# Kernel optimization log

Hardware: AMD Instinct MI355X
Metric: run time of the kernel (lower is better)

Reference implementation:

```python
import jax, jax.numpy as jnp
import numpy as np

CLASS_NUM = 80
REG_MAX = 16
INPUT_W, INPUT_H = 640, 640
BS, MAXB, TOPK = 16, 20, 10
ALPHA, BETA = 0.5, 6.0
EPS = 1e-9
BOX_W, CLS_W, DFL_W = 7.5, 0.5, 1.5


def _make_anchors(strides=(8, 16, 32), offset=0.5):
    pts, svec = [], []
    for s in strides:
        h, w = INPUT_H // s, INPUT_W // s
        sx = np.arange(w, dtype=np.float32) + offset
        sy = np.arange(h, dtype=np.float32) + offset
        gy, gx = np.meshgrid(sy, sx, indexing="ij")
        pts.append(np.stack([gx, gy], -1).reshape(-1, 2))
        svec.append(np.full((h * w, 1), s, dtype=np.float32))
    return jnp.asarray(np.concatenate(pts)), jnp.asarray(np.concatenate(svec))


def _xywh2xyxy(x):
    xy, wh = x[..., :2], x[..., 2:4]
    return jnp.concatenate([xy - wh / 2, xy + wh / 2], -1)


def _ciou(b1, b2, eps=1e-7):
    # b1, b2: (..., 4) in xyxy; standard ultralytics CIoU (h gets +eps -> safe for zero boxes)
    b1x1, b1y1, b1x2, b1y2 = (b1[..., i] for i in range(4))
    b2x1, b2y1, b2x2, b2y2 = (b2[..., i] for i in range(4))
    w1, h1 = b1x2 - b1x1, b1y2 - b1y1 + eps
    w2, h2 = b2x2 - b2x1, b2y2 - b2y1 + eps
    inter = (jnp.minimum(b1x2, b2x2) - jnp.maximum(b1x1, b2x1)).clip(0) * \
            (jnp.minimum(b1y2, b2y2) - jnp.maximum(b1y1, b2y1)).clip(0)
    union = w1 * h1 + w2 * h2 - inter + eps
    iou = inter / union
    cw = jnp.maximum(b1x2, b2x2) - jnp.minimum(b1x1, b2x1)
    ch = jnp.maximum(b1y2, b2y2) - jnp.minimum(b1y1, b2y1)
    c2 = cw * cw + ch * ch + eps
    rho2 = ((b2x1 + b2x2 - b1x1 - b1x2) ** 2 + (b2y1 + b2y2 - b1y1 - b1y2) ** 2) / 4.0
    v = (4.0 / np.pi ** 2) * (jnp.arctan(w2 / h2) - jnp.arctan(w1 / h1)) ** 2
    alpha = jax.lax.stop_gradient(v / (v - iou + (1.0 + eps)))
    return iou - (rho2 / c2 + v * alpha)


def _assigner(pd_scores, pd_bboxes, anc_points, gt_labels, gt_bboxes, mask_gt):
    # Task-aligned assignment. pd_scores (b,na,nc) sigmoided, pd_bboxes (b,na,4), mask_gt (b,M,1).
    b, na, nc = pd_scores.shape
    M = gt_bboxes.shape[1]
    f32 = pd_scores.dtype
    # anchors whose center lies inside each gt box -> (b,M,na)
    lt = anc_points[None, None] - gt_bboxes[:, :, None, :2]
    rb = gt_bboxes[:, :, None, 2:] - anc_points[None, None]
    mask_in_gts = (jnp.concatenate([lt, rb], -1).min(-1) > EPS).astype(f32)
    mask = mask_in_gts * mask_gt  # (b,M,na)
    labels = gt_labels[..., 0].astype(jnp.int32)  # (b,M)
    idx = jnp.broadcast_to(labels[:, :, None], (b, M, na))
    bbox_scores = jnp.take_along_axis(pd_scores.transpose(0, 2, 1), idx, axis=1) * mask  # (b,M,na)
    overlaps = jnp.clip(_ciou(gt_bboxes[:, :, None, :], pd_bboxes[:, None, :, :]), 0) * mask
    align = bbox_scores ** ALPHA * overlaps ** BETA  # (b,M,na)
    # topk candidates per gt along anchors
    _, topk_idxs = jax.lax.top_k(align, TOPK)  # (b,M,TOPK)
    valid = jnp.broadcast_to(mask_gt > 0, (b, M, TOPK))
    idxs = jnp.where(valid, topk_idxs, 0).reshape(b * M, TOPK)
    cnt = jnp.zeros((b * M, na), f32).at[jnp.arange(b * M)[:, None], idxs].add(
        valid.reshape(b * M, TOPK).astype(f32)).reshape(b, M, na)
    mask_topk = jnp.where(cnt > 1, 0.0, cnt)
    mask_pos = mask_topk * mask  # (b,M,na)
    # anchors claimed by multiple gts keep only the highest-overlap gt
    fg = mask_pos.sum(-2)  # (b,na)
    is_max = jax.nn.one_hot(overlaps.argmax(1), M, dtype=f32).transpose(0, 2, 1)  # (b,M,na)
    mask_pos = jnp.where(fg[:, None, :] > 1, is_max, mask_pos)
    fg_mask = mask_pos.sum(-2)  # (b,na)
    target_gt_idx = mask_pos.argmax(-2)  # (b,na)
    flat_idx = target_gt_idx + jnp.arange(b)[:, None] * M
    t_labels = labels.reshape(-1)[flat_idx]  # (b,na)
    t_bboxes = gt_bboxes.reshape(-1, 4)[flat_idx]  # (b,na,4)
    t_scores = jax.nn.one_hot(t_labels, nc, dtype=f32) * (fg_mask[..., None] > 0).astype(f32)
    # normalize by task-aligned metric
    align = align * mask_pos
    pos_align = align.max(axis=-1, keepdims=True)  # (b,M,1)
    pos_overlaps = (overlaps * mask_pos).max(axis=-1, keepdims=True)
    norm = (align * pos_overlaps / (pos_align + EPS)).max(axis=-2)[..., None]  # (b,na,1)
    return t_bboxes, t_scores * norm, fg_mask


def yolo_loss(feat0, feat1, feat2, annotations):
    rm = REG_MAX
    preds = []
    for f in (feat0, feat1, feat2):
        b, c, h, w = f.shape
        preds.append(f.reshape(b, c, h * w).transpose(0, 2, 1))
    preds = jnp.concatenate(preds, 1)  # (b, 8400, 4*rm+nc)
    pred_regs = preds[..., :4 * rm]
    pred_scores = preds[..., 4 * rm:]
    anc_points, stride_scales = _make_anchors()  # (8400,2), (8400,1)
    b, a, _ = pred_regs.shape
    # DFL decode: softmax over 16 bins, expectation with proj = arange(16)
    dist = jax.nn.softmax(pred_regs.reshape(b, a, 4, rm), -1) @ jnp.arange(rm, dtype=preds.dtype)
    pred_bboxes = jnp.concatenate([anc_points - dist[..., :2], anc_points + dist[..., 2:]], -1)
    # gt processing: fixed MAXB boxes per image, zero padded (ann_process equivalent)
    res = annotations.reshape(b, MAXB, 6)[..., 1:]
    scales = jnp.array([INPUT_W, INPUT_H, INPUT_W, INPUT_H], dtype=res.dtype)
    gt_bboxes = _xywh2xyxy(res[..., :4]) * scales
    gt_labels = res[..., 4:]
    gt_mask = (gt_bboxes.sum(2, keepdims=True) > 0).astype(res.dtype)
    t_bboxes, t_scores, fg_mask = _assigner(
        jax.lax.stop_gradient(jax.nn.sigmoid(pred_scores)),
        jax.lax.stop_gradient(pred_bboxes * stride_scales),
        anc_points * stride_scales, gt_labels, gt_bboxes, gt_mask)
    tss = jnp.maximum(t_scores.sum(), 1.0)
    # cls: BCE-with-logits, sum / target_scores_sum
    x, t = pred_scores, t_scores
    bce = jnp.maximum(x, 0) - x * t + jnp.log1p(jnp.exp(-jnp.abs(x)))
    loss_cls = bce.sum() / tss
    # box (CIoU) + DFL, weighted by per-anchor score sum on fg anchors
    t_bboxes = t_bboxes / stride_scales
    weight = t_scores.sum(-1) * fg_mask  # (b,na); zero off fg
    iou = _ciou(pred_bboxes, t_bboxes)
    loss_box = jnp.sum((1.0 - iou) * weight) / tss
    target_ltrb = jnp.clip(
        jnp.concatenate([anc_points - t_bboxes[..., :2], t_bboxes[..., 2:] - anc_points], -1),
        0.0, (rm - 1) - 0.01)  # (b,na,4)
    logp = jax.nn.log_softmax(pred_regs.reshape(b, a, 4, rm), -1)
    tl = target_ltrb.astype(jnp.int32)
    wl = (tl + 1).astype(logp.dtype) - target_ltrb
    ce_tl = -jnp.take_along_axis(logp, tl[..., None], -1)[..., 0]
    ce_tr = -jnp.take_along_axis(logp, tl[..., None] + 1, -1)[..., 0]
    dfl = (ce_tl * wl + ce_tr * (1.0 - wl)).mean(-1)  # (b,na)
    loss_dfl = jnp.sum(dfl * weight) / tss
    loss = jnp.stack([loss_box * BOX_W, loss_cls * CLS_W, loss_dfl * DFL_W])
    return loss.sum(), jax.lax.stop_gradient(loss)


def setup_inputs() -> dict:
    key = jax.random.key(0)
    k1, k2, k3, k4, k5, k6 = jax.random.split(key, 6)
    C = 4 * REG_MAX + CLASS_NUM  # 144
    feat0 = jax.random.normal(k1, (BS, C, 80, 80), jnp.float32)
    feat1 = jax.random.normal(k2, (BS, C, 40, 40), jnp.float32)
    feat2 = jax.random.normal(k3, (BS, C, 20, 20), jnp.float32)
    # annotations rows: [batch_idx, x, y, w, h (normalized), cls]; zero-padded to MAXB per image
    cx = jax.random.uniform(k4, (BS, MAXB), minval=0.15, maxval=0.85)
    cy = jax.random.uniform(jax.random.fold_in(k4, 1), (BS, MAXB), minval=0.15, maxval=0.85)
    w = jax.random.uniform(k5, (BS, MAXB), minval=0.05, maxval=0.3)
    h = jax.random.uniform(jax.random.fold_in(k5, 1), (BS, MAXB), minval=0.05, maxval=0.3)
    cls = jax.random.randint(k6, (BS, MAXB), 0, CLASS_NUM).astype(jnp.float32)
    counts = jax.random.randint(jax.random.fold_in(k6, 1), (BS,), 5, MAXB + 1)
    valid = (jnp.arange(MAXB)[None, :] < counts[:, None]).astype(jnp.float32)
    bidx = jnp.broadcast_to(jnp.arange(BS, dtype=jnp.float32)[:, None], (BS, MAXB))
    ann = jnp.stack([bidx, cx * valid, cy * valid, w * valid, h * valid, cls * valid], -1)
    return {"feat0": feat0, "feat1": feat1, "feat2": feat2,
            "annotations": ann.reshape(BS * MAXB, 6)}


def reference(feat0, feat1, feat2, annotations):
    return yolo_loss(feat0, feat1, feat2, annotations)
```

## Files before the change

kernel.cpp:

```cpp
#include <hip/hip_runtime.h>

#define NA_TOT 8400
#define A0 6400
#define A1 8000
#define NC_TOT 144
#define BSZ 16
#define MB 20
#define TOPKN 10
#define NCLS 80


__device__ __forceinline__ const float* feat_sel(const float* f0, const float* f1,
                                                 const float* f2, int a, int& hw, int& pos) {
  if (a < A0) { hw = 6400; pos = a;      return f0; }
  if (a < A1) { hw = 1600; pos = a - A0; return f1; }
  hw = 400; pos = a - A1; return f2;
}

__device__ __forceinline__ void anchor_geom(int a, float& stride, float& ax, float& ay) {
  int pos, w;
  if (a < A0)      { pos = a;      w = 80; stride = 8.f;  }
  else if (a < A1) { pos = a - A0; w = 40; stride = 16.f; }
  else             { pos = a - A1; w = 20; stride = 32.f; }
  int y = pos / w, x = pos - y * w;
  ax = (float)x + 0.5f; ay = (float)y + 0.5f;
}

__device__ __forceinline__ float ciou_f(float b1x1, float b1y1, float b1x2, float b1y2,
                                        float b2x1, float b2y1, float b2x2, float b2y2) {
  const float eps = 1e-7f;
  float w1 = b1x2 - b1x1, h1 = b1y2 - b1y1 + eps;
  float w2 = b2x2 - b2x1, h2 = b2y2 - b2y1 + eps;
  float iw = fminf(b1x2, b2x2) - fmaxf(b1x1, b2x1);
  float ih = fminf(b1y2, b2y2) - fmaxf(b1y1, b2y1);
  float inter = fmaxf(iw, 0.f) * fmaxf(ih, 0.f);
  float uni = w1 * h1 + w2 * h2 - inter + eps;
  float iou = inter / uni;
  float cw = fmaxf(b1x2, b2x2) - fminf(b1x1, b2x1);
  float ch = fmaxf(b1y2, b2y2) - fminf(b1y1, b2y1);
  float c2 = cw * cw + ch * ch + eps;
  float dx = b2x1 + b2x2 - b1x1 - b1x2;
  float dy = b2y1 + b2y2 - b1y1 - b1y2;
  float rho2 = (dx * dx + dy * dy) * 0.25f;
  float dat = atanf(w2 / h2) - atanf(w1 / h1);
  float v = 0.4052847345693511f * dat * dat;
  float alpha = v / (v - iou + (1.f + eps));
  return iou - (rho2 / c2 + v * alpha);
}

__device__ __forceinline__ bool better(float v1, int i1, float v2, int i2) {
  return (v1 > v2) || (v1 == v2 && i1 < i2);
}


#define PREP_TILES 132

__global__ __launch_bounds__(256) void k_prep(const float* __restrict__ f0,
                                              const float* __restrict__ f1,
                                              const float* __restrict__ f2,
                                              float4* __restrict__ pbox,
                                              float4* __restrict__ lse4,
                                              double* __restrict__ acc) {
  __shared__ float s_d[64][5];
  __shared__ float s_ls[64][5];
  __shared__ float s_red[4];
  int tile = blockIdx.x % PREP_TILES;
  int b    = blockIdx.x / PREP_TILES;
  int w = threadIdx.x >> 6, l = threadIdx.x & 63;
  int a = tile * 64 + l;
  float bce = 0.f;
  if (a < NA_TOT) {
    int hw, pos; const float* f = feat_sel(f0, f1, f2, a, hw, pos);
    const float* base = f + (size_t)b * NC_TOT * hw + pos;
    float v[16]; float m = -1e30f;
#pragma unroll
    for (int i = 0; i < 16; i++) { v[i] = base[(size_t)(w * 16 + i) * hw]; m = fmaxf(m, v[i]); }
    float s = 0.f, ws = 0.f;
#pragma unroll
    for (int i = 0; i < 16; i++) { float e = expf(v[i] - m); s += e; ws += e * (float)i; }
    s_d[l][w]  = ws / s;
    s_ls[l][w] = m + logf(s);
#pragma unroll
    for (int j = 0; j < 20; j++) {
      float x = base[(size_t)(64 + w * 20 + j) * hw];
      bce += fmaxf(x, 0.f) + log1pf(expf(-fabsf(x)));
    }
  }
  for (int o = 32; o > 0; o >>= 1) bce += __shfl_down(bce, o, 64);
  if (l == 0) s_red[w] = bce;
  __syncthreads();
  if (threadIdx.x == 0)
    atomicAdd(&acc[0], (double)(s_red[0] + s_red[1] + s_red[2] + s_red[3]));
  if (threadIdx.x < 64 && a < NA_TOT) {
    float stride, ax, ay; anchor_geom(a, stride, ax, ay);
    int idx = b * NA_TOT + a;
    pbox[idx] = make_float4(ax - s_d[l][0], ay - s_d[l][1], ax + s_d[l][2], ay + s_d[l][3]);
    lse4[idx] = make_float4(s_ls[l][0], s_ls[l][1], s_ls[l][2], s_ls[l][3]);
  }
}


__global__ __launch_bounds__(256) void k_align(const float* __restrict__ f0,
                                               const float* __restrict__ f1,
                                               const float* __restrict__ f2,
                                               const float* __restrict__ ann,
                                               const float4* __restrict__ pbox,
                                               float* __restrict__ alg,
                                               float* __restrict__ ovl,
                                               unsigned char* __restrict__ sel) {
  int idx = blockIdx.x * 256 + threadIdx.x;
  int bm = idx / NA_TOT, a = idx - bm * NA_TOT;
  int b = bm / MB;
  const float* g = ann + (size_t)bm * 6;
  float cx = g[1], cy = g[2], w_ = g[3], h_ = g[4];
  float gx1 = (cx - w_ * 0.5f) * 640.f, gy1 = (cy - h_ * 0.5f) * 640.f;
  float gx2 = (cx + w_ * 0.5f) * 640.f, gy2 = (cy + h_ * 0.5f) * 640.f;
  int label = (int)g[5];
  bool valid = (gx1 + gy1 + gx2 + gy2) > 0.f;

  float stride, ax, ay; anchor_geom(a, stride, ax, ay);
  float axp = ax * stride, ayp = ay * stride;
  float mn = fminf(fminf(axp - gx1, ayp - gy1), fminf(gx2 - axp, gy2 - ayp));
  float al = 0.f, ov = 0.f;
  if (valid && mn > 1e-9f) {
    float4 pb = pbox[b * NA_TOT + a];
    float px1 = pb.x * stride, py1 = pb.y * stride;
    float px2 = pb.z * stride, py2 = pb.w * stride;
    ov = fmaxf(ciou_f(gx1, gy1, gx2, gy2, px1, py1, px2, py2), 0.f);
    int hw, pos; const float* f = feat_sel(f0, f1, f2, a, hw, pos);
    float xs = f[((size_t)b * NC_TOT + 64 + label) * hw + pos];
    float sg = 1.f / (1.f + expf(-xs));
    float o2 = ov * ov;
    al = sqrtf(sg) * (o2 * o2 * o2);
  }
  alg[idx] = al;
  ovl[idx] = ov;
  sel[idx] = 0;
}


__global__ __launch_bounds__(256) void k_topk(const float* __restrict__ alg,
                                              const float* __restrict__ ann,
                                              unsigned char* __restrict__ sel) {
  __shared__ float s_v[4];
  __shared__ int   s_i[4];
  __shared__ float s_bv;
  __shared__ int   s_bi;
  __shared__ int   s_top[TOPKN];

  int bm = blockIdx.x;
  const float* row = alg + (size_t)bm * NA_TOT;
  const float* g = ann + (size_t)bm * 6;
  float cx = g[1], cy = g[2], w_ = g[3], h_ = g[4];
  float gx1 = (cx - w_ * 0.5f) * 640.f, gy1 = (cy - h_ * 0.5f) * 640.f;
  float gx2 = (cx + w_ * 0.5f) * 640.f, gy2 = (cy + h_ * 0.5f) * 640.f;
  bool valid = (gx1 + gy1 + gx2 + gy2) > 0.f;

  float lv[TOPKN]; int li[TOPKN];
#pragma unroll
  for (int k = 0; k < TOPKN; k++) { lv[k] = -1.f; li[k] = 0x7fffffff; }
  for (int a = threadIdx.x; a < NA_TOT; a += 256) {
    float v = row[a];
    if (better(v, a, lv[TOPKN - 1], li[TOPKN - 1])) {
      float cv = v; int ci = a;
#pragma unroll
      for (int k = 0; k < TOPKN; k++) {
        bool bb = better(cv, ci, lv[k], li[k]);
        float tv = bb ? cv : lv[k]; int ti = bb ? ci : li[k];
        cv = bb ? lv[k] : cv;       ci = bb ? li[k] : ci;
        lv[k] = tv; li[k] = ti;
      }
    }
  }

  int wv = threadIdx.x >> 6;
  for (int k = 0; k < TOPKN; k++) {
    float bv = lv[0]; int bi = li[0];
    for (int o = 32; o > 0; o >>= 1) {
      float xv = __shfl_down(bv, o, 64);
      int   xi = __shfl_down(bi, o, 64);
      if (better(xv, xi, bv, bi)) { bv = xv; bi = xi; }
    }
    if ((threadIdx.x & 63) == 0) { s_v[wv] = bv; s_i[wv] = bi; }
    __syncthreads();
    if (threadIdx.x == 0) {
      float fv = s_v[0]; int fi = s_i[0];
      for (int q = 1; q < 4; q++)
        if (better(s_v[q], s_i[q], fv, fi)) { fv = s_v[q]; fi = s_i[q]; }
      s_top[k] = fi; s_bv = fv; s_bi = fi;
    }
    __syncthreads();
    if (lv[0] == s_bv && li[0] == s_bi) {
#pragma unroll
      for (int q = 0; q < TOPKN - 1; q++) { lv[q] = lv[q + 1]; li[q] = li[q + 1]; }
      lv[TOPKN - 1] = -1.f; li[TOPKN - 1] = 0x7fffffff;
    }
    __syncthreads();
  }

  if (threadIdx.x < TOPKN && valid) {
    int a = s_top[threadIdx.x];
    float stride, ax, ay; anchor_geom(a, stride, ax, ay);
    float axp = ax * stride, ayp = ay * stride;
    float mn = fminf(fminf(axp - gx1, ayp - gy1), fminf(gx2 - axp, gy2 - ayp));
    if (mn > 1e-9f) sel[(size_t)bm * NA_TOT + a] = 1;
  }
}


__global__ __launch_bounds__(256) void k_resolve(const float* __restrict__ alg,
                                                 const float* __restrict__ ovl,
                                                 const unsigned char* __restrict__ sel,
                                                 unsigned char* __restrict__ tgt,
                                                 unsigned char* __restrict__ fgm,
                                                 unsigned int* __restrict__ pos_a,
                                                 unsigned int* __restrict__ pos_o) {
  int idx = blockIdx.x * 256 + threadIdx.x;
  int b = idx / NA_TOT, a = idx - b * NA_TOT;
  size_t col = (size_t)b * MB * NA_TOT + a;
  int fg = 0, first = -1;
#pragma unroll
  for (int m = 0; m < MB; m++) {
    int v = sel[col + (size_t)m * NA_TOT];
    fg += v;
    if (v && first < 0) first = m;
  }
  int t, f;
  if (fg > 1) {
    float bv = ovl[col]; int bm_ = 0;
#pragma unroll
    for (int m = 1; m < MB; m++) {
      float v = ovl[col + (size_t)m * NA_TOT];
      if (v > bv) { bv = v; bm_ = m; }
    }
    t = bm_; f = 1;
  } else {
    t = (first >= 0) ? first : 0;
    f = fg;
  }
  tgt[idx] = (unsigned char)t;
  fgm[idx] = (unsigned char)f;
  if (f) {
    int bm = b * MB + t;
    float al = alg[(size_t)bm * NA_TOT + a];
    float ov = ovl[(size_t)bm * NA_TOT + a];
    atomicMax(&pos_a[bm], __float_as_uint(al));
    atomicMax(&pos_o[bm], __float_as_uint(ov));
  }
}


__global__ __launch_bounds__(256) void k_loss(const float* __restrict__ f0,
                                              const float* __restrict__ f1,
                                              const float* __restrict__ f2,
                                              const float* __restrict__ ann,
                                              const float4* __restrict__ pbox,
                                              const float4* __restrict__ lse4,
                                              const float* __restrict__ alg,
                                              const unsigned char* __restrict__ tgt,
                                              const unsigned char* __restrict__ fgm,
                                              const unsigned int* __restrict__ pos_a,
                                              const unsigned int* __restrict__ pos_o,
                                              double* __restrict__ acc) {
  int idx = blockIdx.x * 256 + threadIdx.x;
  int b = idx / NA_TOT, a = idx - b * NA_TOT;
  float c_cls = 0.f, c_box = 0.f, c_dfl = 0.f, c_tss = 0.f;

  if (fgm[idx]) {
    int t = tgt[idx];
    int bm = b * MB + t;
    float al = alg[(size_t)bm * NA_TOT + a];
    float norm = al * __uint_as_float(pos_o[bm]) / (__uint_as_float(pos_a[bm]) + 1e-9f);

    const float* g = ann + (size_t)bm * 6;
    float stride, ax, ay; anchor_geom(a, stride, ax, ay);
    int hw, pos; const float* f = feat_sel(f0, f1, f2, a, hw, pos);
    const float* base = f + (size_t)b * NC_TOT * hw + pos;

    int label = (int)g[5];
    float xs = base[(size_t)(64 + label) * hw];
    c_cls = xs * norm;
    c_tss = norm;

    float cx = g[1], cy = g[2], w_ = g[3], h_ = g[4];
    float inv = 1.f / stride;
    float tx1 = (cx - w_ * 0.5f) * 640.f * inv, ty1 = (cy - h_ * 0.5f) * 640.f * inv;
    float tx2 = (cx + w_ * 0.5f) * 640.f * inv, ty2 = (cy + h_ * 0.5f) * 640.f * inv;

    float4 pb = pbox[idx];
    float iou = ciou_f(pb.x, pb.y, pb.z, pb.w, tx1, ty1, tx2, ty2);
    c_box = (1.f - iou) * norm;

    float4 ls = lse4[idx];
    float ltv[4] = { ax - tx1, ay - ty1, tx2 - ax, ty2 - ay };
    float lsa[4] = { ls.x, ls.y, ls.z, ls.w };
    float dfl = 0.f;
#pragma unroll
    for (int g4 = 0; g4 < 4; g4++) {
      float tv = fminf(fmaxf(ltv[g4], 0.f), 14.99f);
      int   tl = (int)tv;
      float wl = (float)(tl + 1) - tv;
      float xl = base[(size_t)(g4 * 16 + tl) * hw];
      float xr = base[(size_t)(g4 * 16 + tl + 1) * hw];
      dfl += (lsa[g4] - xl) * wl + (lsa[g4] - xr) * (1.f - wl);
    }
    c_dfl = dfl * 0.25f * norm;
  }

  for (int o = 32; o > 0; o >>= 1) {
    c_cls += __shfl_down(c_cls, o, 64);
    c_box += __shfl_down(c_box, o, 64);
    c_dfl += __shfl_down(c_dfl, o, 64);
    c_tss += __shfl_down(c_tss, o, 64);
  }
  __shared__ float sh[4][4];
  int wv = threadIdx.x >> 6;
  if ((threadIdx.x & 63) == 0) { sh[wv][0] = c_cls; sh[wv][1] = c_box; sh[wv][2] = c_dfl; sh[wv][3] = c_tss; }
  __syncthreads();
  if (threadIdx.x == 0) {
    float t0 = sh[0][0] + sh[1][0] + sh[2][0] + sh[3][0];
    float t1 = sh[0][1] + sh[1][1] + sh[2][1] + sh[3][1];
    float t2 = sh[0][2] + sh[1][2] + sh[2][2] + sh[3][2];
    float t3 = sh[0][3] + sh[1][3] + sh[2][3] + sh[3][3];
    atomicAdd(&acc[0], -(double)t0);
    atomicAdd(&acc[1],  (double)t1);
    atomicAdd(&acc[2],  (double)t2);
    atomicAdd(&acc[3],  (double)t3);
  }
}


__global__ void k_finish(const double* __restrict__ acc, float* __restrict__ out) {
  double tss = acc[3]; if (tss < 1.0) tss = 1.0;
  float lb = (float)(acc[1] / tss) * 7.5f;
  float lc = (float)(acc[0] / tss) * 0.5f;
  float ld = (float)(acc[2] / tss) * 1.5f;
  out[0] = lb + lc + ld;
  out[1] = lb;
  out[2] = lc;
  out[3] = ld;
}


extern "C" void kernel_launch(void* const* d_in, const int* in_sizes, int n_in,
                              void* d_out, int out_size, void* d_ws, size_t ws_size,
                              hipStream_t stream) {
  const float* f0  = (const float*)d_in[0];
  const float* f1  = (const float*)d_in[1];
  const float* f2  = (const float*)d_in[2];
  const float* ann = (const float*)d_in[3];

  char* p = (char*)d_ws;
  size_t off = 0;
  double* acc = (double*)(p + off);               off += 64;
  unsigned int* pos_a = (unsigned int*)(p + off); off += (size_t)BSZ * MB * 4;
  unsigned int* pos_o = (unsigned int*)(p + off); off += (size_t)BSZ * MB * 4;
  size_t zero_bytes = off;
  float4* pbox = (float4*)(p + off);              off += (size_t)BSZ * NA_TOT * 16;
  float4* lse4 = (float4*)(p + off);              off += (size_t)BSZ * NA_TOT * 16;
  float* alg = (float*)(p + off);                 off += (size_t)BSZ * MB * NA_TOT * 4;
  float* ovl = (float*)(p + off);                 off += (size_t)BSZ * MB * NA_TOT * 4;
  unsigned char* sel = (unsigned char*)(p + off); off += (size_t)BSZ * MB * NA_TOT;
  unsigned char* tgt = (unsigned char*)(p + off); off += (size_t)BSZ * NA_TOT;
  unsigned char* fgm = (unsigned char*)(p + off); off += (size_t)BSZ * NA_TOT;

  hipMemsetAsync(acc, 0, zero_bytes, stream);

  const int NBLK = (BSZ * NA_TOT) / 256;
  k_prep<<<BSZ * PREP_TILES, 256, 0, stream>>>(f0, f1, f2, pbox, lse4, acc);
  k_align<<<(BSZ * MB * NA_TOT) / 256, 256, 0, stream>>>(f0, f1, f2, ann, pbox, alg, ovl, sel);
  k_topk<<<BSZ * MB, 256, 0, stream>>>(alg, ann, sel);
  k_resolve<<<NBLK, 256, 0, stream>>>(alg, ovl, sel, tgt, fgm, pos_a, pos_o);
  k_loss<<<NBLK, 256, 0, stream>>>(f0, f1, f2, ann, pbox, lse4, alg, tgt, fgm, pos_a, pos_o, acc);
  k_finish<<<1, 1, 0, stream>>>(acc, (float*)d_out);
}
```

Baseline: 203.1 us.

## Use per-anchor bitmask for top-k selection and precompute GT box terms

Replaces the per-(gt,anchor) byte selection array with a per-anchor 32-bit mask set by atomicOr in top-k, so resolve reads one word and uses popcount/ffs instead of scanning 20 rows. A new tiny kernel precomputes GT box corners, area, atan of aspect, label and validity, which align and top-k then load as two float4s. The BCE sum is rewritten to multiply (1+exp(-|x|)) terms and take one log, using fast __expf. This cuts memory traffic and transcendental work, at the cost of an extra launch, atomics, and a possible overflow or precision change in the product-of-terms BCE.

After: 191.7 us. -5.6%, faster.

```diff
diff --git a/kernel.cpp b/kernel.cpp
--- a/kernel.cpp
+++ b/kernel.cpp
@@ -53,6 +53,22 @@
 }
 
 
+__global__ void k_gtt(const float* __restrict__ ann, float* __restrict__ gtt) {
+  int bm = threadIdx.x;
+  const float* g = ann + bm * 6;
+  float cx = g[1], cy = g[2], w_ = g[3], h_ = g[4];
+  float gx1 = (cx - w_ * 0.5f) * 640.f, gy1 = (cy - h_ * 0.5f) * 640.f;
+  float gx2 = (cx + w_ * 0.5f) * 640.f, gy2 = (cy + h_ * 0.5f) * 640.f;
+  float w1 = gx2 - gx1, h1 = gy2 - gy1 + 1e-7f;
+  float* o = gtt + bm * 8;
+  o[0] = gx1; o[1] = gy1; o[2] = gx2; o[3] = gy2;
+  o[4] = w1 * h1;
+  o[5] = atanf(w1 / h1);
+  o[6] = g[5];
+  o[7] = ((gx1 + gy1 + gx2 + gy2) > 0.f) ? 1.f : 0.f;
+}
+
+
 #define PREP_TILES 132
 
 __global__ __launch_bounds__(256) void k_prep(const float* __restrict__ f0,
@@ -60,10 +76,12 @@
                                               const float* __restrict__ f2,
                                               float4* __restrict__ pbox,
                                               float4* __restrict__ lse4,
+                                              unsigned int* __restrict__ selmask,
                                               double* __restrict__ acc) {
   __shared__ float s_d[64][5];
   __shared__ float s_ls[64][5];
   __shared__ float s_red[4];
+
   int tile = blockIdx.x % PREP_TILES;
   int b    = blockIdx.x / PREP_TILES;
   int w = threadIdx.x >> 6, l = threadIdx.x & 63;
@@ -72,19 +90,26 @@
   if (a < NA_TOT) {
     int hw, pos; const float* f = feat_sel(f0, f1, f2, a, hw, pos);
     const float* base = f + (size_t)b * NC_TOT * hw + pos;
+    int co = w * 16 * hw;
     float v[16]; float m = -1e30f;
 #pragma unroll
-    for (int i = 0; i < 16; i++) { v[i] = base[(size_t)(w * 16 + i) * hw]; m = fmaxf(m, v[i]); }
+    for (int i = 0; i < 16; i++) { v[i] = base[co + i * hw]; m = fmaxf(m, v[i]); }
     float s = 0.f, ws = 0.f;
 #pragma unroll
     for (int i = 0; i < 16; i++) { float e = expf(v[i] - m); s += e; ws += e * (float)i; }
     s_d[l][w]  = ws / s;
     s_ls[l][w] = m + logf(s);
-#pragma unroll
-    for (int j = 0; j < 20; j++) {
-      float x = base[(size_t)(64 + w * 20 + j) * hw];
-      bce += fmaxf(x, 0.f) + log1pf(expf(-fabsf(x)));
-    }
+    int cc = (64 + w * 20) * hw;
+    float relu = 0.f, pr0 = 1.f, pr1 = 1.f;
+#pragma unroll
+    for (int j = 0; j < 20; j += 2) {
+      float x0 = base[cc + j * hw];
+      float x1 = base[cc + (j + 1) * hw];
+      relu += fmaxf(x0, 0.f) + fmaxf(x1, 0.f);
+      pr0 *= 1.f + __expf(-fabsf(x0));
+      pr1 *= 1.f + __expf(-fabsf(x1));
+    }
+    bce = relu + logf(pr0 * pr1);
   }
   for (int o = 32; o > 0; o >>= 1) bce += __shfl_down(bce, o, 64);
   if (l == 0) s_red[w] = bce;
@@ -96,6 +121,7 @@
     int idx = b * NA_TOT + a;
     pbox[idx] = make_float4(ax - s_d[l][0], ay - s_d[l][1], ax + s_d[l][2], ay + s_d[l][3]);
     lse4[idx] = make_float4(s_ls[l][0], s_ls[l][1], s_ls[l][2], s_ls[l][3]);
+    selmask[idx] = 0u;
   }
 }
 
@@ -103,30 +129,46 @@
 __global__ __launch_bounds__(256) void k_align(const float* __restrict__ f0,
                                                const float* __restrict__ f1,
                                                const float* __restrict__ f2,
-                                               const float* __restrict__ ann,
+                                               const float* __restrict__ gtt,
                                                const float4* __restrict__ pbox,
                                                float* __restrict__ alg,
-                                               float* __restrict__ ovl,
-                                               unsigned char* __restrict__ sel) {
+                                               float* __restrict__ ovl) {
   int idx = blockIdx.x * 256 + threadIdx.x;
   int bm = idx / NA_TOT, a = idx - bm * NA_TOT;
   int b = bm / MB;
-  const float* g = ann + (size_t)bm * 6;
-  float cx = g[1], cy = g[2], w_ = g[3], h_ = g[4];
-  float gx1 = (cx - w_ * 0.5f) * 640.f, gy1 = (cy - h_ * 0.5f) * 640.f;
-  float gx2 = (cx + w_ * 0.5f) * 640.f, gy2 = (cy + h_ * 0.5f) * 640.f;
-  int label = (int)g[5];
-  bool valid = (gx1 + gy1 + gx2 + gy2) > 0.f;
+  float4 t0 = *(const float4*)(gtt + bm * 8);
+  float4 t1 = *(const float4*)(gtt + bm * 8 + 4);
+  float gx1 = t0.x, gy1 = t0.y, gx2 = t0.z, gy2 = t0.w;
+  float area1 = t1.x, atn1 = t1.y;
+  int label = (int)t1.z;
+  bool valid = t1.w > 0.f;
 
   float stride, ax, ay; anchor_geom(a, stride, ax, ay);
   float axp = ax * stride, ayp = ay * stride;
   float mn = fminf(fminf(axp - gx1, ayp - gy1), fminf(gx2 - axp, gy2 - ayp));
   float al = 0.f, ov = 0.f;
   if (valid && mn > 1e-9f) {
+    const float eps = 1e-7f;
     float4 pb = pbox[b * NA_TOT + a];
     float px1 = pb.x * stride, py1 = pb.y * stride;
     float px2 = pb.z * stride, py2 = pb.w * stride;
-    ov = fmaxf(ciou_f(gx1, gy1, gx2, gy2, px1, py1, px2, py2), 0.f);
+    float w2 = px2 - px1, h2 = py2 - py1 + eps;
+    float iw = fminf(gx2, px2) - fmaxf(gx1, px1);
+    float ih = fminf(gy2, py2) - fmaxf(gy1, py1);
+    float inter = fmaxf(iw, 0.f) * fmaxf(ih, 0.f);
+    float uni = area1 + w2 * h2 - inter + eps;
+    float iou = inter / uni;
+    float cw = fmaxf(gx2, px2) - fminf(gx1, px1);
+    float ch = fmaxf(gy2, py2) - fminf(gy1, py1);
+    float c2 = cw * cw + ch * ch + eps;
+    float dx = px1 + px2 - gx1 - gx2;
+    float dy = py1 + py2 - gy1 - gy2;
+    float rho2 = (dx * dx + dy * dy) * 0.25f;
+    float dat = atanf(w2 / h2) - atn1;
+    float v = 0.4052847345693511f * dat * dat;
+    float alpha = v / (v - iou + (1.f + eps));
+    ov = fmaxf(iou - (rho2 / c2 + v * alpha), 0.f);
+
     int hw, pos; const float* f = feat_sel(f0, f1, f2, a, hw, pos);
     float xs = f[((size_t)b * NC_TOT + 64 + label) * hw + pos];
     float sg = 1.f / (1.f + expf(-xs));
@@ -135,13 +177,12 @@
   }
   alg[idx] = al;
   ovl[idx] = ov;
-  sel[idx] = 0;
 }
 
 
 __global__ __launch_bounds__(256) void k_topk(const float* __restrict__ alg,
-                                              const float* __restrict__ ann,
-                                              unsigned char* __restrict__ sel) {
+                                              const float* __restrict__ gtt,
+                                              unsigned int* __restrict__ selmask) {
   __shared__ float s_v[4];
   __shared__ int   s_i[4];
   __shared__ float s_bv;
@@ -149,12 +190,12 @@
   __shared__ int   s_top[TOPKN];
 
   int bm = blockIdx.x;
+  int b = bm / MB, m = bm - b * MB;
   const float* row = alg + (size_t)bm * NA_TOT;
-  const float* g = ann + (size_t)bm * 6;
-  float cx = g[1], cy = g[2], w_ = g[3], h_ = g[4];
-  float gx1 = (cx - w_ * 0.5f) * 640.f, gy1 = (cy - h_ * 0.5f) * 640.f;
-  float gx2 = (cx + w_ * 0.5f) * 640.f, gy2 = (cy + h_ * 0.5f) * 640.f;
-  bool valid = (gx1 + gy1 + gx2 + gy2) > 0.f;
+  float4 t0 = *(const float4*)(gtt + bm * 8);
+  float4 t1 = *(const float4*)(gtt + bm * 8 + 4);
+  float gx1 = t0.x, gy1 = t0.y, gx2 = t0.z, gy2 = t0.w;
+  bool valid = t1.w > 0.f;
 
   float lv[TOPKN]; int li[TOPKN];
 #pragma unroll
@@ -203,14 +244,14 @@
     float stride, ax, ay; anchor_geom(a, stride, ax, ay);
     float axp = ax * stride, ayp = ay * stride;
     float mn = fminf(fminf(axp - gx1, ayp - gy1), fminf(gx2 - axp, gy2 - ayp));
-    if (mn > 1e-9f) sel[(size_t)bm * NA_TOT + a] = 1;
+    if (mn > 1e-9f) atomicOr(&selmask[b * NA_TOT + a], 1u << m);
   }
 }
 
 
 __global__ __launch_bounds__(256) void k_resolve(const float* __restrict__ alg,
                                                  const float* __restrict__ ovl,
-                                                 const unsigned char* __restrict__ sel,
+                                                 const unsigned int* __restrict__ selmask,
                                                  unsigned char* __restrict__ tgt,
                                                  unsigned char* __restrict__ fgm,
                                                  unsigned int* __restrict__ pos_a,
@@ -218,13 +259,8 @@
   int idx = blockIdx.x * 256 + threadIdx.x;
   int b = idx / NA_TOT, a = idx - b * NA_TOT;
   size_t col = (size_t)b * MB * NA_TOT + a;
-  int fg = 0, first = -1;
-#pragma unroll
-  for (int m = 0; m < MB; m++) {
-    int v = sel[col + (size_t)m * NA_TOT];
-    fg += v;
-    if (v && first < 0) first = m;
-  }
+  unsigned int mask = selmask[idx];
+  int fg = __popc(mask);
   int t, f;
   if (fg > 1) {
     float bv = ovl[col]; int bm_ = 0;
@@ -235,7 +271,7 @@
     }
     t = bm_; f = 1;
   } else {
-    t = (first >= 0) ? first : 0;
+    t = mask ? (__ffs(mask) - 1) : 0;
     f = fg;
   }
   tgt[idx] = (unsigned char)t;
@@ -360,17 +396,19 @@
   float4* lse4 = (float4*)(p + off);              off += (size_t)BSZ * NA_TOT * 16;
   float* alg = (float*)(p + off);                 off += (size_t)BSZ * MB * NA_TOT * 4;
   float* ovl = (float*)(p + off);                 off += (size_t)BSZ * MB * NA_TOT * 4;
-  unsigned char* sel = (unsigned char*)(p + off); off += (size_t)BSZ * MB * NA_TOT;
+  unsigned int* selmask = (unsigned int*)(p + off); off += (size_t)BSZ * NA_TOT * 4;
+  float* gtt = (float*)(p + off);                 off += (size_t)BSZ * MB * 8 * 4;
   unsigned char* tgt = (unsigned char*)(p + off); off += (size_t)BSZ * NA_TOT;
   unsigned char* fgm = (unsigned char*)(p + off); off += (size_t)BSZ * NA_TOT;
 
   hipMemsetAsync(acc, 0, zero_bytes, stream);
 
   const int NBLK = (BSZ * NA_TOT) / 256;
-  k_prep<<<BSZ * PREP_TILES, 256, 0, stream>>>(f0, f1, f2, pbox, lse4, acc);
-  k_align<<<(BSZ * MB * NA_TOT) / 256, 256, 0, stream>>>(f0, f1, f2, ann, pbox, alg, ovl, sel);
-  k_topk<<<BSZ * MB, 256, 0, stream>>>(alg, ann, sel);
-  k_resolve<<<NBLK, 256, 0, stream>>>(alg, ovl, sel, tgt, fgm, pos_a, pos_o);
+  k_gtt<<<1, BSZ * MB, 0, stream>>>(ann, gtt);
+  k_prep<<<BSZ * PREP_TILES, 256, 0, stream>>>(f0, f1, f2, pbox, lse4, selmask, acc);
+  k_align<<<(BSZ * MB * NA_TOT) / 256, 256, 0, stream>>>(f0, f1, f2, gtt, pbox, alg, ovl);
+  k_topk<<<BSZ * MB, 256, 0, stream>>>(alg, gtt, selmask);
+  k_resolve<<<NBLK, 256, 0, stream>>>(alg, ovl, selmask, tgt, fgm, pos_a, pos_o);
   k_loss<<<NBLK, 256, 0, stream>>>(f0, f1, f2, ann, pbox, lse4, alg, tgt, fgm, pos_a, pos_o, acc);
   k_finish<<<1, 1, 0, stream>>>(acc, (float*)d_out);
 }
```
